# Optimization experiments

Measured on AMD Instinct MI355X. Metric: run time of the kernel, lower is better.

The kernel has to match this reference:

```python
import jax, jax.numpy as jnp
import numpy as np

RESO = 128

def _prefix_a3(layer, off0):
    # a3[0]=off0; a3[i]=a3[i-1]+2*layer[i-1]+2*layer[i]
    t = jnp.concatenate([jnp.zeros((1,), layer.dtype), 2.0 * layer[:-1] + 2.0 * layer[1:]])
    return off0 + jnp.cumsum(t)

def _prefix_a6(layer, a3):
    # a6[0]=0; a6[i]=a6[i-1]+3*layer[i-1]+layer[i]+2*a3[i-1]
    s = jnp.concatenate([jnp.zeros((1,), layer.dtype), 3.0 * layer[:-1] + layer[1:] + 2.0 * a3[:-1]])
    return jnp.cumsum(s)

def _decode(idx, reso):
    iz = idx % reso                 # selects xLayer channels (0,3)
    iy = (idx // reso) % reso       # selects yLayer channels (1,4)
    ix = idx // (reso * reso)       # selects zLayer channels (2,5)
    return ix, iy, iz

def setup_inputs() -> dict:
    key = jax.random.key(0)
    k1, k2, k3, k4 = jax.random.split(key, 4)
    N = 4194304
    reso = RESO
    ncells = reso ** 3
    renderPointList = jax.random.normal(k1, (N, 3), dtype=jnp.float32) * reso * 0.3 + reso * 0.5
    sdfPointList = jax.random.normal(k2, (N, 3), dtype=jnp.float32) * reso * 0.3 + reso * 0.5
    renderIndexList = jax.random.randint(k3, (N,), 0, ncells, dtype=jnp.int64) if jax.config.jax_enable_x64 else jax.random.randint(k3, (N,), 0, ncells).astype(jnp.int32)
    sdfIndexList = jax.random.randint(k4, (N,), 0, ncells).astype(renderIndexList.dtype)
    xLayer = jnp.ones((reso,), dtype=jnp.float32)
    yLayer = jnp.ones((reso,), dtype=jnp.float32)
    zLayer = jnp.ones((reso,), dtype=jnp.float32)
    c = 1.0 - reso
    offset = jnp.array([2 * c, 2 * c, 2 * c, 3 * c * c - float(reso) ** 2], dtype=jnp.float32)
    return {"renderPointList": renderPointList, "renderIndexList": renderIndexList,
            "sdfPointList": sdfPointList, "sdfIndexList": sdfIndexList,
            "xLayer": xLayer, "yLayer": yLayer, "zLayer": zLayer, "offset": offset}

def reference(renderPointList, renderIndexList, sdfPointList, sdfIndexList, xLayer, yLayer, zLayer, offset):
    reso = xLayer.shape[0]
    xA3 = _prefix_a3(xLayer, offset[0])
    yA4 = _prefix_a3(yLayer, offset[1])
    zA5 = _prefix_a3(zLayer, offset[2])
    xA6 = _prefix_a6(xLayer, xA3)
    yA6 = _prefix_a6(yLayer, yA4)
    zA6 = _prefix_a6(zLayer, zA5)

    # ---- SDF evaluation ----
    ix, iy, iz = _decode(sdfIndexList, reso)
    px, py, pz = sdfPointList[:, 0], sdfPointList[:, 1], sdfPointList[:, 2]
    a0 = xLayer[iz] * px
    a1 = yLayer[iy] * py
    a2 = zLayer[ix] * pz
    a3 = xA3[iz]
    a4 = yA4[iy]
    a5 = zA5[ix]
    a6 = offset[3] + xA6[iz] + yA6[iy] + zA6[ix]
    num = (a0 + a3) * px + (a1 + a4) * py + (a2 + a5) * pz + a6
    den = jnp.sqrt((2 * a0 + a3) ** 2 + (2 * a1 + a4) ** 2 + (2 * a2 + a5) ** 2)
    sdfList = num / den / reso

    # ---- Normal evaluation ----
    jx, jy, jz = _decode(renderIndexList, reso)
    rx, ry, rz = renderPointList[:, 0], renderPointList[:, 1], renderPointList[:, 2]
    nx = 2 * xLayer[jz] * rx + xA3[jz]
    ny = 2 * yLayer[jy] * ry + yA4[jy]
    nz = 2 * zLayer[jx] * rz + zA5[jx]
    n = jnp.stack([nx, ny, nz], axis=1)  # [N,3]
    norm = jnp.sqrt(jnp.sum(n * n, axis=1, keepdims=True))
    normalList = n / jnp.maximum(norm, 1e-12)
    return (sdfList, normalList)
```

## Files before the change

kernel.cpp:

```cpp
#include <hip/hip_runtime.h>

#define RESO 128

__global__ __launch_bounds__(256) void fused_kernel(
    const float* __restrict__ renderPts, const int* __restrict__ renderIdx,
    const float* __restrict__ sdfPts,    const int* __restrict__ sdfIdx,
    const float* __restrict__ xL, const float* __restrict__ yL,
    const float* __restrict__ zL, const float* __restrict__ off,
    float* __restrict__ sdfOut, float* __restrict__ nrmOut, int N)
{
    __shared__ float tab[9][RESO];
    __shared__ float s_a3[RESO];
    __shared__ float s_tmp[4];

    const int tid  = threadIdx.x;
    const int lane = tid & 63;
    const int wave = tid >> 6;

    for (int ax = 0; ax < 3; ++ax) {
        const float* L = (ax == 0) ? xL : (ax == 1) ? yL : zL;
        float li = 0.f, lim1 = 0.f, v = 0.f, w = 0.f, a3v = 0.f;
        if (tid < RESO) {
            li   = L[tid];
            lim1 = (tid > 0) ? L[tid - 1] : 0.f;
            v = (tid == 0) ? 0.f : 2.f * lim1 + 2.f * li;
            #pragma unroll
            for (int o = 1; o < 64; o <<= 1) {
                float u = __shfl_up(v, o, 64);
                if (lane >= o) v += u;
            }
            if (lane == 63) s_tmp[wave] = v;
        }
        __syncthreads();
        if (tid < RESO) {
            if (wave == 1) v += s_tmp[0];
            a3v = off[ax] + v;
            s_a3[tid] = a3v;
        }
        __syncthreads();
        if (tid < RESO) {
            const float a3m1 = (tid > 0) ? s_a3[tid - 1] : 0.f;
            w = (tid == 0) ? 0.f : 3.f * lim1 + li + 2.f * a3m1;
            #pragma unroll
            for (int o = 1; o < 64; o <<= 1) {
                float u = __shfl_up(w, o, 64);
                if (lane >= o) w += u;
            }
            if (lane == 63) s_tmp[2 + wave] = w;
        }
        __syncthreads();
        if (tid < RESO) {
            if (wave == 1) w += s_tmp[2];
            tab[ax][tid]     = li;
            tab[3 + ax][tid] = a3v;
            tab[6 + ax][tid] = w;
        }
        __syncthreads();
    }

    const float off3 = off[3];
    const int Ng = N >> 2;
    const int t  = blockIdx.x * blockDim.x + tid;

    if (t < Ng) {
        const int4   sid = ((const int4*)sdfIdx)[t];
        const float4 sp0 = ((const float4*)sdfPts)[3 * t + 0];
        const float4 sp1 = ((const float4*)sdfPts)[3 * t + 1];
        const float4 sp2 = ((const float4*)sdfPts)[3 * t + 2];
        const float px[4] = {sp0.x, sp0.w, sp1.z, sp2.y};
        const float py[4] = {sp0.y, sp1.x, sp1.w, sp2.z};
        const float pz[4] = {sp0.z, sp1.y, sp2.x, sp2.w};
        const int  ids[4] = {sid.x, sid.y, sid.z, sid.w};

        float sv[4];
        #pragma unroll
        for (int k = 0; k < 4; ++k) {
            const int id = ids[k];
            const int iz = id & 127;
            const int iy = (id >> 7) & 127;
            const int ix = (id >> 14) & 127;
            const float a0 = tab[0][iz] * px[k];
            const float a1 = tab[1][iy] * py[k];
            const float a2 = tab[2][ix] * pz[k];
            const float a3 = tab[3][iz];
            const float a4 = tab[4][iy];
            const float a5 = tab[5][ix];
            const float a6 = off3 + tab[6][iz] + tab[7][iy] + tab[8][ix];
            const float num = (a0 + a3) * px[k] + (a1 + a4) * py[k] + (a2 + a5) * pz[k] + a6;
            const float dx = 2.f * a0 + a3;
            const float dy = 2.f * a1 + a4;
            const float dz = 2.f * a2 + a5;
            const float den = sqrtf(dx * dx + dy * dy + dz * dz);
            sv[k] = num / den * (1.0f / (float)RESO);
        }
        ((float4*)sdfOut)[t] = make_float4(sv[0], sv[1], sv[2], sv[3]);

        const int4   rid = ((const int4*)renderIdx)[t];
        const float4 rp0 = ((const float4*)renderPts)[3 * t + 0];
        const float4 rp1 = ((const float4*)renderPts)[3 * t + 1];
        const float4 rp2 = ((const float4*)renderPts)[3 * t + 2];
        const float rx[4] = {rp0.x, rp0.w, rp1.z, rp2.y};
        const float ry[4] = {rp0.y, rp1.x, rp1.w, rp2.z};
        const float rz[4] = {rp0.z, rp1.y, rp2.x, rp2.w};
        const int  jds[4] = {rid.x, rid.y, rid.z, rid.w};

        float nx[4], ny[4], nz[4];
        #pragma unroll
        for (int k = 0; k < 4; ++k) {
            const int id = jds[k];
            const int jz = id & 127;
            const int jy = (id >> 7) & 127;
            const int jx = (id >> 14) & 127;
            float x = 2.f * tab[0][jz] * rx[k] + tab[3][jz];
            float y = 2.f * tab[1][jy] * ry[k] + tab[4][jy];
            float z = 2.f * tab[2][jx] * rz[k] + tab[5][jx];
            const float nrm = sqrtf(x * x + y * y + z * z);
            const float inv = 1.0f / fmaxf(nrm, 1e-12f);
            nx[k] = x * inv; ny[k] = y * inv; nz[k] = z * inv;
        }
        float4* no = (float4*)nrmOut;
        no[3 * t + 0] = make_float4(nx[0], ny[0], nz[0], nx[1]);
        no[3 * t + 1] = make_float4(ny[1], nz[1], nx[2], ny[2]);
        no[3 * t + 2] = make_float4(nz[2], nx[3], ny[3], nz[3]);
    }

    const int rem = N & 3;
    if (rem && t == Ng) {
        for (int r = 0; r < rem; ++r) {
            const int i = 4 * Ng + r;
            {
                const int id = sdfIdx[i];
                const int iz = id & 127, iy = (id >> 7) & 127, ix = (id >> 14) & 127;
                const float px_ = sdfPts[3 * i], py_ = sdfPts[3 * i + 1], pz_ = sdfPts[3 * i + 2];
                const float a0 = tab[0][iz] * px_;
                const float a1 = tab[1][iy] * py_;
                const float a2 = tab[2][ix] * pz_;
                const float a3 = tab[3][iz], a4 = tab[4][iy], a5 = tab[5][ix];
                const float a6 = off3 + tab[6][iz] + tab[7][iy] + tab[8][ix];
                const float num = (a0 + a3) * px_ + (a1 + a4) * py_ + (a2 + a5) * pz_ + a6;
                const float dx = 2.f * a0 + a3, dy = 2.f * a1 + a4, dz = 2.f * a2 + a5;
                sdfOut[i] = num / sqrtf(dx * dx + dy * dy + dz * dz) * (1.0f / (float)RESO);
            }
            {
                const int id = renderIdx[i];
                const int jz = id & 127, jy = (id >> 7) & 127, jx = (id >> 14) & 127;
                const float rx_ = renderPts[3 * i], ry_ = renderPts[3 * i + 1], rz_ = renderPts[3 * i + 2];
                float x = 2.f * tab[0][jz] * rx_ + tab[3][jz];
                float y = 2.f * tab[1][jy] * ry_ + tab[4][jy];
                float z = 2.f * tab[2][jx] * rz_ + tab[5][jx];
                const float inv = 1.0f / fmaxf(sqrtf(x * x + y * y + z * z), 1e-12f);
                nrmOut[3 * i] = x * inv; nrmOut[3 * i + 1] = y * inv; nrmOut[3 * i + 2] = z * inv;
            }
        }
    }
}

extern "C" void kernel_launch(void* const* d_in, const int* in_sizes, int n_in,
                              void* d_out, int out_size, void* d_ws, size_t ws_size,
                              hipStream_t stream)
{
    const float* renderPts = (const float*)d_in[0];
    const int*   renderIdx = (const int*)d_in[1];
    const float* sdfPts    = (const float*)d_in[2];
    const int*   sdfIdx    = (const int*)d_in[3];
    const float* xL        = (const float*)d_in[4];
    const float* yL        = (const float*)d_in[5];
    const float* zL        = (const float*)d_in[6];
    const float* off       = (const float*)d_in[7];

    float* out = (float*)d_out;
    const int N = in_sizes[1];

    const int Ng    = N >> 2;
    const int rem   = N & 3;
    const int total = Ng + (rem ? 1 : 0);
    int grid = (total + 255) / 256;
    if (grid < 1) grid = 1;

    fused_kernel<<<grid, 256, 0, stream>>>(renderPts, renderIdx, sdfPts, sdfIdx,
                                           xL, yL, zL, off, out, out + N, N);
}
```

Measured before the change: 189.2 us.

## Hoist prefix-scan tables into a separate kernel and use a persistent grid-stride loop

```diff
diff --git a/kernel.cpp b/kernel.cpp
--- a/kernel.cpp
+++ b/kernel.cpp
@@ -1,155 +1,176 @@
 #include <hip/hip_runtime.h>
 
 #define RESO 128
+
+__global__ __launch_bounds__(128) void scan_kernel(
+    const float* __restrict__ xL, const float* __restrict__ yL,
+    const float* __restrict__ zL, const float* __restrict__ off,
+    float* __restrict__ ws)
+{
+    __shared__ float s_tmp[4];
+    __shared__ float s_a3[RESO];
+
+    const int tid  = threadIdx.x;
+    const int lane = tid & 63;
+    const int wave = tid >> 6;
+
+    for (int ax = 0; ax < 3; ++ax) {
+        const float* L = (ax == 0) ? xL : (ax == 1) ? yL : zL;
+        const float li   = L[tid];
+        const float lim1 = (tid > 0) ? L[tid - 1] : 0.f;
+
+        float v = (tid == 0) ? 0.f : 2.f * lim1 + 2.f * li;
+        #pragma unroll
+        for (int o = 1; o < 64; o <<= 1) {
+            float u = __shfl_up(v, o, 64);
+            if (lane >= o) v += u;
+        }
+        if (lane == 63) s_tmp[wave] = v;
+        __syncthreads();
+        if (wave == 1) v += s_tmp[0];
+        const float a3v = off[ax] + v;
+        s_a3[tid] = a3v;
+        __syncthreads();
+
+        const float a3m1 = (tid > 0) ? s_a3[tid - 1] : 0.f;
+        float w = (tid == 0) ? 0.f : 3.f * lim1 + li + 2.f * a3m1;
+        #pragma unroll
+        for (int o = 1; o < 64; o <<= 1) {
+            float u = __shfl_up(w, o, 64);
+            if (lane >= o) w += u;
+        }
+        if (lane == 63) s_tmp[2 + wave] = w;
+        __syncthreads();
+        if (wave == 1) w += s_tmp[2];
+
+        ws[ax * RESO + tid]       = li;
+        ws[(3 + ax) * RESO + tid] = a3v;
+        ws[(6 + ax) * RESO + tid] = w;
+        __syncthreads();
+    }
+}
 
 __global__ __launch_bounds__(256) void fused_kernel(
     const float* __restrict__ renderPts, const int* __restrict__ renderIdx,
     const float* __restrict__ sdfPts,    const int* __restrict__ sdfIdx,
-    const float* __restrict__ xL, const float* __restrict__ yL,
-    const float* __restrict__ zL, const float* __restrict__ off,
+    const float* __restrict__ ws,        const float* __restrict__ off,
     float* __restrict__ sdfOut, float* __restrict__ nrmOut, int N)
 {
-    __shared__ float tab[9][RESO];
-    __shared__ float s_a3[RESO];
-    __shared__ float s_tmp[4];
-
-    const int tid  = threadIdx.x;
-    const int lane = tid & 63;
-    const int wave = tid >> 6;
-
-    for (int ax = 0; ax < 3; ++ax) {
-        const float* L = (ax == 0) ? xL : (ax == 1) ? yL : zL;
-        float li = 0.f, lim1 = 0.f, v = 0.f, w = 0.f, a3v = 0.f;
-        if (tid < RESO) {
-            li   = L[tid];
-            lim1 = (tid > 0) ? L[tid - 1] : 0.f;
-            v = (tid == 0) ? 0.f : 2.f * lim1 + 2.f * li;
+    __shared__ float4 tabS[3][RESO];
+    __shared__ float2 tabR[3][RESO];
+
+    const int tid = threadIdx.x;
+    if (tid < RESO) {
+        #pragma unroll
+        for (int ax = 0; ax < 3; ++ax) {
+            const float L  = ws[ax * RESO + tid];
+            const float a3 = ws[(3 + ax) * RESO + tid];
+            const float a6 = ws[(6 + ax) * RESO + tid];
+            tabS[ax][tid] = make_float4(L, a3, a6, 0.f);
+            tabR[ax][tid] = make_float2(L, a3);
+        }
+    }
+    __syncthreads();
+
+    const float off3 = off[3];
+    const int Ng  = N >> 2;
+    const int rem = N & 3;
+    const int total = Ng + (rem ? 1 : 0);
+    const int stride = gridDim.x * blockDim.x;
+
+    for (int t = blockIdx.x * blockDim.x + tid; t < total; t += stride) {
+        if (t < Ng) {
+            const int4   sid = ((const int4*)sdfIdx)[t];
+            const float4 sp0 = ((const float4*)sdfPts)[3 * t + 0];
+            const float4 sp1 = ((const float4*)sdfPts)[3 * t + 1];
+            const float4 sp2 = ((const float4*)sdfPts)[3 * t + 2];
+            const float px[4] = {sp0.x, sp0.w, sp1.z, sp2.y};
+            const float py[4] = {sp0.y, sp1.x, sp1.w, sp2.z};
+            const float pz[4] = {sp0.z, sp1.y, sp2.x, sp2.w};
+            const int  ids[4] = {sid.x, sid.y, sid.z, sid.w};
+
+            float sv[4];
             #pragma unroll
-            for (int o = 1; o < 64; o <<= 1) {
-                float u = __shfl_up(v, o, 64);
-                if (lane >= o) v += u;
+            for (int k = 0; k < 4; ++k) {
+                const int id = ids[k];
+                const float4 tx = tabS[0][id & 127];
+                const float4 ty = tabS[1][(id >> 7) & 127];
+                const float4 tz = tabS[2][(id >> 14) & 127];
+                const float a0 = tx.x * px[k];
+                const float a1 = ty.x * py[k];
+                const float a2 = tz.x * pz[k];
+                const float a6 = off3 + tx.z + ty.z + tz.z;
+                const float num = (a0 + tx.y) * px[k] + (a1 + ty.y) * py[k]
+                                + (a2 + tz.y) * pz[k] + a6;
+                const float dx = 2.f * a0 + tx.y;
+                const float dy = 2.f * a1 + ty.y;
+                const float dz = 2.f * a2 + tz.y;
+                const float d2 = dx * dx + dy * dy + dz * dz;
+                sv[k] = num * __builtin_amdgcn_rsqf(d2) * (1.0f / (float)RESO);
             }
-            if (lane == 63) s_tmp[wave] = v;
-        }
-        __syncthreads();
-        if (tid < RESO) {
-            if (wave == 1) v += s_tmp[0];
-            a3v = off[ax] + v;
-            s_a3[tid] = a3v;
-        }
-        __syncthreads();
-        if (tid < RESO) {
-            const float a3m1 = (tid > 0) ? s_a3[tid - 1] : 0.f;
-            w = (tid == 0) ? 0.f : 3.f * lim1 + li + 2.f * a3m1;
+            ((float4*)sdfOut)[t] = make_float4(sv[0], sv[1], sv[2], sv[3]);
+
+            const int4   rid = ((const int4*)renderIdx)[t];
+            const float4 rp0 = ((const float4*)renderPts)[3 * t + 0];
+            const float4 rp1 = ((const float4*)renderPts)[3 * t + 1];
+            const float4 rp2 = ((const float4*)renderPts)[3 * t + 2];
+            const float rx[4] = {rp0.x, rp0.w, rp1.z, rp2.y};
+            const float ry[4] = {rp0.y, rp1.x, rp1.w, rp2.z};
+            const float rz[4] = {rp0.z, rp1.y, rp2.x, rp2.w};
+            const int  jds[4] = {rid.x, rid.y, rid.z, rid.w};
+
+            float nx[4], ny[4], nz[4];
             #pragma unroll
-            for (int o = 1; o < 64; o <<= 1) {
-                float u = __shfl_up(w, o, 64);
-                if (lane >= o) w += u;
+            for (int k = 0; k < 4; ++k) {
+                const int id = jds[k];
+                const float2 ux = tabR[0][id & 127];
+                const float2 uy = tabR[1][(id >> 7) & 127];
+                const float2 uz = tabR[2][(id >> 14) & 127];
+                const float x = 2.f * ux.x * rx[k] + ux.y;
+                const float y = 2.f * uy.x * ry[k] + uy.y;
+                const float z = 2.f * uz.x * rz[k] + uz.y;
+                const float n2 = x * x + y * y + z * z;
+                const float inv = __builtin_amdgcn_rsqf(fmaxf(n2, 1e-24f));
+                nx[k] = x * inv; ny[k] = y * inv; nz[k] = z * inv;
             }
-            if (lane == 63) s_tmp[2 + wave] = w;
-        }
-        __syncthreads();
-        if (tid < RESO) {
-            if (wave == 1) w += s_tmp[2];
-            tab[ax][tid]     = li;
-            tab[3 + ax][tid] = a3v;
-            tab[6 + ax][tid] = w;
-        }
-        __syncthreads();
-    }
-
-    const float off3 = off[3];
-    const int Ng = N >> 2;
-    const int t  = blockIdx.x * blockDim.x + tid;
-
-    if (t < Ng) {
-        const int4   sid = ((const int4*)sdfIdx)[t];
-        const float4 sp0 = ((const float4*)sdfPts)[3 * t + 0];
-        const float4 sp1 = ((const float4*)sdfPts)[3 * t + 1];
-        const float4 sp2 = ((const float4*)sdfPts)[3 * t + 2];
-        const float px[4] = {sp0.x, sp0.w, sp1.z, sp2.y};
-        const float py[4] = {sp0.y, sp1.x, sp1.w, sp2.z};
-        const float pz[4] = {sp0.z, sp1.y, sp2.x, sp2.w};
-        const int  ids[4] = {sid.x, sid.y, sid.z, sid.w};
-
-        float sv[4];
-        #pragma unroll
-        for (int k = 0; k < 4; ++k) {
-            const int id = ids[k];
-            const int iz = id & 127;
-            const int iy = (id >> 7) & 127;
-            const int ix = (id >> 14) & 127;
-            const float a0 = tab[0][iz] * px[k];
-            const float a1 = tab[1][iy] * py[k];
-            const float a2 = tab[2][ix] * pz[k];
-            const float a3 = tab[3][iz];
-            const float a4 = tab[4][iy];
-            const float a5 = tab[5][ix];
-            const float a6 = off3 + tab[6][iz] + tab[7][iy] + tab[8][ix];
-            const float num = (a0 + a3) * px[k] + (a1 + a4) * py[k] + (a2 + a5) * pz[k] + a6;
-            const float dx = 2.f * a0 + a3;
-            const float dy = 2.f * a1 + a4;
-            const float dz = 2.f * a2 + a5;
-            const float den = sqrtf(dx * dx + dy * dy + dz * dz);
-            sv[k] = num / den * (1.0f / (float)RESO);
-        }
-        ((float4*)sdfOut)[t] = make_float4(sv[0], sv[1], sv[2], sv[3]);
-
-        const int4   rid = ((const int4*)renderIdx)[t];
-        const float4 rp0 = ((const float4*)renderPts)[3 * t + 0];
-        const float4 rp1 = ((const float4*)renderPts)[3 * t + 1];
-        const float4 rp2 = ((const float4*)renderPts)[3 * t + 2];
-        const float rx[4] = {rp0.x, rp0.w, rp1.z, rp2.y};
-        const float ry[4] = {rp0.y, rp1.x, rp1.w, rp2.z};
-        const float rz[4] = {rp0.z, rp1.y, rp2.x, rp2.w};
-        const int  jds[4] = {rid.x, rid.y, rid.z, rid.w};
-
-        float nx[4], ny[4], nz[4];
-        #pragma unroll
-        for (int k = 0; k < 4; ++k) {
-            const int id = jds[k];
-            const int jz = id & 127;
-            const int jy = (id >> 7) & 127;
-            const int jx = (id >> 14) & 127;
-            float x = 2.f * tab[0][jz] * rx[k] + tab[3][jz];
-            float y = 2.f * tab[1][jy] * ry[k] + tab[4][jy];
-            float z = 2.f * tab[2][jx] * rz[k] + tab[5][jx];
-            const float nrm = sqrtf(x * x + y * y + z * z);
-            const float inv = 1.0f / fmaxf(nrm, 1e-12f);
-            nx[k] = x * inv; ny[k] = y * inv; nz[k] = z * inv;
-        }
-        float4* no = (float4*)nrmOut;
-        no[3 * t + 0] = make_float4(nx[0], ny[0], nz[0], nx[1]);
-        no[3 * t + 1] = make_float4(ny[1], nz[1], nx[2], ny[2]);
-        no[3 * t + 2] = make_float4(nz[2], nx[3], ny[3], nz[3]);
-    }
-
-    const int rem = N & 3;
-    if (rem && t == Ng) {
-        for (int r = 0; r < rem; ++r) {
-            const int i = 4 * Ng + r;
-            {
-                const int id = sdfIdx[i];
-                const int iz = id & 127, iy = (id >> 7) & 127, ix = (id >> 14) & 127;
-                const float px_ = sdfPts[3 * i], py_ = sdfPts[3 * i + 1], pz_ = sdfPts[3 * i + 2];
-                const float a0 = tab[0][iz] * px_;
-                const float a1 = tab[1][iy] * py_;
-                const float a2 = tab[2][ix] * pz_;
-                const float a3 = tab[3][iz], a4 = tab[4][iy], a5 = tab[5][ix];
-                const float a6 = off3 + tab[6][iz] + tab[7][iy] + tab[8][ix];
-                const float num = (a0 + a3) * px_ + (a1 + a4) * py_ + (a2 + a5) * pz_ + a6;
-                const float dx = 2.f * a0 + a3, dy = 2.f * a1 + a4, dz = 2.f * a2 + a5;
-                sdfOut[i] = num / sqrtf(dx * dx + dy * dy + dz * dz) * (1.0f / (float)RESO);
-            }
-            {
-                const int id = renderIdx[i];
-                const int jz = id & 127, jy = (id >> 7) & 127, jx = (id >> 14) & 127;
-                const float rx_ = renderPts[3 * i], ry_ = renderPts[3 * i + 1], rz_ = renderPts[3 * i + 2];
-                float x = 2.f * tab[0][jz] * rx_ + tab[3][jz];
-                float y = 2.f * tab[1][jy] * ry_ + tab[4][jy];
-                float z = 2.f * tab[2][jx] * rz_ + tab[5][jx];
-                const float inv = 1.0f / fmaxf(sqrtf(x * x + y * y + z * z), 1e-12f);
-                nrmOut[3 * i] = x * inv; nrmOut[3 * i + 1] = y * inv; nrmOut[3 * i + 2] = z * inv;
+            float4* no = (float4*)nrmOut;
+            no[3 * t + 0] = make_float4(nx[0], ny[0], nz[0], nx[1]);
+            no[3 * t + 1] = make_float4(ny[1], nz[1], nx[2], ny[2]);
+            no[3 * t + 2] = make_float4(nz[2], nx[3], ny[3], nz[3]);
+        } else {
+            for (int r = 0; r < rem; ++r) {
+                const int i = 4 * Ng + r;
+                {
+                    const int id = sdfIdx[i];
+                    const float4 tx = tabS[0][id & 127];
+                    const float4 ty = tabS[1][(id >> 7) & 127];
+                    const float4 tz = tabS[2][(id >> 14) & 127];
+                    const float px_ = sdfPts[3 * i], py_ = sdfPts[3 * i + 1], pz_ = sdfPts[3 * i + 2];
+                    const float a0 = tx.x * px_;
+                    const float a1 = ty.x * py_;
+                    const float a2 = tz.x * pz_;
+                    const float a6 = off3 + tx.z + ty.z + tz.z;
+                    const float num = (a0 + tx.y) * px_ + (a1 + ty.y) * py_
+                                    + (a2 + tz.y) * pz_ + a6;
+                    const float dx = 2.f * a0 + tx.y;
+                    const float dy = 2.f * a1 + ty.y;
+                    const float dz = 2.f * a2 + tz.y;
+                    const float d2 = dx * dx + dy * dy + dz * dz;
+                    sdfOut[i] = num * __builtin_amdgcn_rsqf(d2) * (1.0f / (float)RESO);
+                }
+                {
+                    const int id = renderIdx[i];
+                    const float2 ux = tabR[0][id & 127];
+                    const float2 uy = tabR[1][(id >> 7) & 127];
+                    const float2 uz = tabR[2][(id >> 14) & 127];
+                    const float rx_ = renderPts[3 * i], ry_ = renderPts[3 * i + 1], rz_ = renderPts[3 * i + 2];
+                    const float x = 2.f * ux.x * rx_ + ux.y;
+                    const float y = 2.f * uy.x * ry_ + uy.y;
+                    const float z = 2.f * uz.x * rz_ + uz.y;
+                    const float n2 = x * x + y * y + z * z;
+                    const float inv = __builtin_amdgcn_rsqf(fmaxf(n2, 1e-24f));
+                    nrmOut[3 * i] = x * inv; nrmOut[3 * i + 1] = y * inv; nrmOut[3 * i + 2] = z * inv;
+                }
             }
         }
     }
@@ -168,15 +189,12 @@
     const float* zL        = (const float*)d_in[6];
     const float* off       = (const float*)d_in[7];
 
+    float* ws  = (float*)d_ws;
     float* out = (float*)d_out;
     const int N = in_sizes[1];
 
-    const int Ng    = N >> 2;
-    const int rem   = N & 3;
-    const int total = Ng + (rem ? 1 : 0);
-    int grid = (total + 255) / 256;
-    if (grid < 1) grid = 1;
-
-    fused_kernel<<<grid, 256, 0, stream>>>(renderPts, renderIdx, sdfPts, sdfIdx,
-                                           xL, yL, zL, off, out, out + N, N);
+    scan_kernel<<<1, 128, 0, stream>>>(xL, yL, zL, off, ws);
+
+    fused_kernel<<<2048, 256, 0, stream>>>(renderPts, renderIdx, sdfPts, sdfIdx,
+                                           ws, off, out, out + N, N);
 }
```

Measured after the change: 191.7 us. About the same (+1.4%).
